# Performance work log

Hardware: AMD Instinct MI355X
Metric: run time of the kernel (lower is better)

The kernel has to match this reference:

```python
import jax, jax.numpy as jnp
import numpy as np

B, S, D, H, FF = 2, 2048, 512, 8, 2048
DK = D // H
EPS = 1e-3  # LayerNorm epsilon from the original module


def _layer_norm(x, gamma, beta):
    # biased variance over last dim, eps added inside sqrt (matches torch var_mean unbiased=False)
    mean = jnp.mean(x, axis=-1, keepdims=True)
    var = jnp.mean(jnp.square(x - mean), axis=-1, keepdims=True)
    return gamma * ((x - mean) / jnp.sqrt(var + EPS)) + beta


def setup_inputs() -> dict:
    key = jax.random.key(0)
    ks = jax.random.split(key, 16)
    sc = 0.02
    p = {
        'x': jax.random.normal(ks[0], (B, S, D), dtype=jnp.float32),
        'lengths': jax.random.randint(ks[1], (B,), 1, S + 1, dtype=jnp.int32),
        'Wq': jax.random.normal(ks[2], (D, D), dtype=jnp.float32) * sc,
        'bq': jnp.zeros((D,), dtype=jnp.float32),
        'Wk': jax.random.normal(ks[3], (D, D), dtype=jnp.float32) * sc,
        'bk': jnp.zeros((D,), dtype=jnp.float32),
        'Wv': jax.random.normal(ks[4], (D, D), dtype=jnp.float32) * sc,
        'bv': jnp.zeros((D,), dtype=jnp.float32),
        'Wo': jax.random.normal(ks[5], (D, D), dtype=jnp.float32) * sc,
        'bo': jnp.zeros((D,), dtype=jnp.float32),
        'W1': jax.random.normal(ks[6], (D, FF), dtype=jnp.float32) * sc,
        'b1': jnp.zeros((FF,), dtype=jnp.float32),
        'W2': jax.random.normal(ks[7], (FF, D), dtype=jnp.float32) * sc,
        'b2': jnp.zeros((D,), dtype=jnp.float32),
        'gamma1': jnp.ones((D,), dtype=jnp.float32),
        'beta1': jnp.zeros((D,), dtype=jnp.float32),
        'gamma2': jnp.ones((D,), dtype=jnp.float32),
        'beta2': jnp.zeros((D,), dtype=jnp.float32),
    }
    return p


def reference(x, lengths, Wq, bq, Wk, bk, Wv, bv, Wo, bo, W1, b1, W2, b2, gamma1, beta1, gamma2, beta2):
    neg_inf = jnp.float32(-jnp.inf)
    pos = jnp.arange(S)
    # pad mask: zero out padded token embeddings (create_pad_mask)
    pad = (pos[None, :] < lengths[:, None]).astype(x.dtype)  # (B, S)
    x = x * pad[:, :, None]

    # hand-rolled multi-head attention (NO 1/sqrt(d_k) scaling, matches original)
    q = (x @ Wq + bq).reshape(B, S, H, DK)
    k = (x @ Wk + bk).reshape(B, S, H, DK)
    v = (x @ Wv + bv).reshape(B, S, H, DK)
    scores = jnp.einsum('bshd,bqhd->bhsq', q, k)  # (B, H, S_query, S_key)

    # causal mask: key col j allowed iff j <= query row i
    causal = pos[None, :] <= pos[:, None]  # (S, S)
    # padding mask: key col j allowed iff j < lengths[b]
    keep = causal[None, None, :, :] & (pos[None, None, None, :] < lengths[:, None, None, None])
    scores = jnp.where(keep, scores, neg_inf)
    attn = jax.nn.softmax(scores, axis=-1)  # (B, H, S, S)

    # FAITHFUL to torch.einsum('bhss,bshd->bshd'): repeated 's' takes the DIAGONAL
    diag = jnp.einsum('bhss->bhs', attn)  # (B, H, S)
    weighted = diag.transpose(0, 2, 1)[:, :, :, None] * v  # (B, S, H, DK)
    attn_out = weighted.reshape(B, S, D) @ Wo + bo

    x = _layer_norm(x + attn_out, gamma1, beta1)
    ff = jax.nn.relu(x @ W1 + b1) @ W2 + b2  # dropout is identity in eval
    x = _layer_norm(x + ff, gamma2, beta2)
    return x
```

## Files before the change

kernel.cpp:

```cpp
#include <hip/hip_runtime.h>

#define B_   2
#define S_   2048
#define D_   512
#define H_   8
#define DK_  64
#define FF_  2048
#define EPS_ 1e-3f
#define QS_  1536

typedef __bf16 bf16;
typedef __bf16 bf16x4 __attribute__((ext_vector_type(4)));
typedef __bf16 bf16x8 __attribute__((ext_vector_type(8)));
typedef float  f32x4  __attribute__((ext_vector_type(4)));

__device__ __forceinline__ void gload16(const bf16* g, bf16* l) {
  __builtin_amdgcn_global_load_lds(
      (__attribute__((address_space(1))) void*)g,
      (__attribute__((address_space(3))) void*)l, 16, 0, 0);
}

struct PrepArgs {
  const float* w[4];
  bf16* thi[4];
  bf16* tlo[4];
  int rowOff[4];
  const float* W1; bf16* W1hi; bf16* W1lo;
  const float* W2; bf16* W2hi; bf16* W2lo;
  const float* x; const int* lengths; bf16* xhi; bf16* xlo;
  const float* bq; const float* bk; const float* bv; float* bqkv;
};

__device__ __forceinline__ void transpose_tile(const float* W, int K, int N,
                                               bf16* Thi, bf16* Tlo,
                                               int n0, int k0, int rowOff,
                                               float (*tl)[33], int t) {
  const int tx = t & 31, ty = t >> 5;
#pragma unroll
  for (int r = 0; r < 32; r += 8)
    tl[r + ty][tx] = W[(size_t)(k0 + r + ty) * N + n0 + tx];
  __syncthreads();
#pragma unroll
  for (int r = 0; r < 32; r += 8) {
    const int n = r + ty;
    const float v = tl[tx][n];
    const bf16 h = (bf16)v;
    const size_t o = (size_t)(rowOff + n0 + n) * K + k0 + tx;
    Thi[o] = h;
    Tlo[o] = (bf16)(v - (float)h);
  }
}

__global__ __launch_bounds__(256) void prep_kernel(PrepArgs a) {
  __shared__ float tl[32][33];
  const int id = blockIdx.x;
  const int t = threadIdx.x;
  if (id < 1024) {
    const int wsel = id >> 8, rem = id & 255;
    transpose_tile(a.w[wsel], 512, 512, a.thi[wsel], a.tlo[wsel],
                   (rem & 15) * 32, (rem >> 4) * 32, a.rowOff[wsel], tl, t);
  } else if (id < 2048) {
    const int rem = id - 1024;
    transpose_tile(a.W1, 512, 2048, a.W1hi, a.W1lo,
                   (rem & 63) * 32, (rem >> 6) * 32, 0, tl, t);
  } else if (id < 3072) {
    const int rem = id - 2048;
    transpose_tile(a.W2, 2048, 512, a.W2hi, a.W2lo,
                   (rem & 15) * 32, (rem >> 4) * 32, 0, tl, t);
  } else if (id < 5120) {
    const int idx = (id - 3072) * 256 + t;
    const int d4 = D_ / 4;
    const int s = (idx / d4) & (S_ - 1);
    const int b = idx / (d4 * S_);
    float4 v = reinterpret_cast<const float4*>(a.x)[idx];
    if (s >= a.lengths[b]) { v.x = 0.f; v.y = 0.f; v.z = 0.f; v.w = 0.f; }
    const float vv[4] = {v.x, v.y, v.z, v.w};
    bf16x4 h, l;
#pragma unroll
    for (int c = 0; c < 4; ++c) {
      const bf16 hh = (bf16)vv[c];
      h[c] = hh;
      l[c] = (bf16)(vv[c] - (float)hh);
    }
    reinterpret_cast<bf16x4*>(a.xhi)[idx] = h;
    reinterpret_cast<bf16x4*>(a.xlo)[idx] = l;
  } else {
    const int i = (id - 5120) * 256 + t;
    if (i < 1536)
      a.bqkv[i] = (i < 512) ? a.bq[i] : (i < 1024) ? a.bk[i - 512] : a.bv[i - 1024];
  }
}

enum { EPI_BIAS_RELU = 2, EPI_PART = 4, EPI_QKV = 5 };

template <int EPI, bool SPLIT, int BN>
__global__ __launch_bounds__(256) void gemm_kernel(
    const bf16* __restrict__ Ahi, const bf16* __restrict__ Alo,
    const bf16* __restrict__ Bhi, const bf16* __restrict__ Blo,
    const float* __restrict__ bias,
    float* __restrict__ C, float* __restrict__ C2,
    bf16* __restrict__ Chi, bf16* __restrict__ Clo,
    int K, int ldc, int nx, int mn, int ksplit) {
  constexpr int NR = BN / 32;
  __shared__ __align__(16) bf16 As[2][128][32];
  __shared__ __align__(16) bf16 Bs[2][BN][32];
  const int t = threadIdx.x;

  const int nwg = gridDim.x;
  const int chunk = nwg >> 3;
  const int virt = (blockIdx.x & 7) * chunk + (blockIdx.x >> 3);
  const int s = virt / mn;
  const int v2 = virt - s * mn;
  const int m0 = (v2 / nx) * 128, n0 = (v2 % nx) * BN;
  const int kb = s * ksplit;

  const int lane = t & 63, wv = t >> 6;
  const int fr = lane & 15, fg = lane >> 4;
  const int wm = (wv >> 1) * 64, wn = (wv & 1) * (BN / 2);
  const int sr = lane >> 2, sslot = lane & 3;

  f32x4 acc[4][NR] = {};

  const bf16* gAh = Ahi + (size_t)m0 * K + kb;
  const bf16* gAl = Alo + (size_t)m0 * K + kb;
  const bf16* gBh = Bhi + (size_t)n0 * K + kb;
  const bf16* gBl = Blo + (size_t)n0 * K + kb;

  for (int k0 = 0; k0 < ksplit; k0 += 32) {
#pragma unroll
    for (int q = 0; q < 2; ++q) {
      const int r = wv * 32 + q * 16 + sr;
      const size_t go = (size_t)r * K + k0 + sslot * 8;
      gload16(gAh + go, &As[0][wv * 32 + q * 16][0]);
      gload16(gAl + go, &As[1][wv * 32 + q * 16][0]);
    }
    if constexpr (BN == 128) {
#pragma unroll
      for (int q = 0; q < 2; ++q) {
        const int r = wv * 32 + q * 16 + sr;
        const size_t go = (size_t)r * K + k0 + sslot * 8;
        gload16(gBh + go, &Bs[0][wv * 32 + q * 16][0]);
        gload16(gBl + go, &Bs[1][wv * 32 + q * 16][0]);
      }
    } else {
      const int r = wv * 16 + sr;
      const size_t go = (size_t)r * K + k0 + sslot * 8;
      gload16(gBh + go, &Bs[0][wv * 16][0]);
      gload16(gBl + go, &Bs[1][wv * 16][0]);
    }
    __syncthreads();

    bf16x8 ah[4], al[4], bh[NR], bl[NR];
#pragma unroll
    for (int m = 0; m < 4; ++m) {
      const int r = wm + m * 16 + fr;
      ah[m] = *reinterpret_cast<const bf16x8*>(&As[0][r][fg * 8]);
      al[m] = *reinterpret_cast<const bf16x8*>(&As[1][r][fg * 8]);
    }
#pragma unroll
    for (int n = 0; n < NR; ++n) {
      const int r = wn + n * 16 + fr;
      bh[n] = *reinterpret_cast<const bf16x8*>(&Bs[0][r][fg * 8]);
      bl[n] = *reinterpret_cast<const bf16x8*>(&Bs[1][r][fg * 8]);
    }
#pragma unroll
    for (int m = 0; m < 4; ++m)
#pragma unroll
      for (int n = 0; n < NR; ++n) {
        acc[m][n] = __builtin_amdgcn_mfma_f32_16x16x32_bf16(bh[n], ah[m], acc[m][n], 0, 0, 0);
        acc[m][n] = __builtin_amdgcn_mfma_f32_16x16x32_bf16(bl[n], ah[m], acc[m][n], 0, 0, 0);
        acc[m][n] = __builtin_amdgcn_mfma_f32_16x16x32_bf16(bh[n], al[m], acc[m][n], 0, 0, 0);
      }
    __syncthreads();
  }

  float* __restrict__ Cw = (s == 0) ? C : C2;
#pragma unroll
  for (int m = 0; m < 4; ++m) {
    const int row = m0 + wm + m * 16 + fr;
#pragma unroll
    for (int n = 0; n < NR; ++n) {
      const int col = n0 + wn + n * 16 + fg * 4;
      f32x4 v = acc[m][n];
      if constexpr (EPI != EPI_PART) {
        const f32x4 b4 = *reinterpret_cast<const f32x4*>(bias + col);
#pragma unroll
        for (int c = 0; c < 4; ++c) v[c] += b4[c];
      }
      if constexpr (EPI == EPI_BIAS_RELU) {
#pragma unroll
        for (int c = 0; c < 4; ++c) v[c] = fmaxf(v[c], 0.f);
      }
      if constexpr (EPI == EPI_QKV) {
        if (col < 1024) {
          bf16x4 h, l;
#pragma unroll
          for (int c = 0; c < 4; ++c) {
            const bf16 hh = (bf16)v[c];
            h[c] = hh;
            l[c] = (bf16)(v[c] - (float)hh);
          }
          *reinterpret_cast<bf16x4*>(&Chi[(size_t)row * 1024 + col]) = h;
          *reinterpret_cast<bf16x4*>(&Clo[(size_t)row * 1024 + col]) = l;
        } else {
          *reinterpret_cast<f32x4*>(&C[(size_t)row * D_ + col - 1024]) = v;
        }
      } else if constexpr (SPLIT) {
        bf16x4 h, l;
#pragma unroll
        for (int c = 0; c < 4; ++c) {
          const bf16 hh = (bf16)v[c];
          h[c] = hh;
          l[c] = (bf16)(v[c] - (float)hh);
        }
        *reinterpret_cast<bf16x4*>(&Chi[(size_t)row * ldc + col]) = h;
        *reinterpret_cast<bf16x4*>(&Clo[(size_t)row * ldc + col]) = l;
      } else {
        *reinterpret_cast<f32x4*>(&Cw[(size_t)row * ldc + col]) = v;
      }
    }
  }
}

__global__ __launch_bounds__(256) void attn_part_kernel(
    const bf16* __restrict__ qk_hi, const bf16* __restrict__ qk_lo,
    const int* __restrict__ lengths,
    float* __restrict__ pm, float* __restrict__ pl, float* __restrict__ pd) {
  __shared__ __align__(16) bf16 Qh[64][72], Ql[64][72];
  __shared__ __align__(16) bf16 Kh[64][72], Kl[64][72];
  const int t = threadIdx.x;
  const int lane = t & 63, wv = t >> 6;
  const int fr = lane & 15, fg = lane >> 4;
  const int bh = blockIdx.y;
  const int bb = bh >> 3, h = bh & 7;

  const int p = blockIdx.x;
  int a = (int)sqrtf((float)p);
  while ((a + 1) * (a + 1) <= p) ++a;
  while (a * a > p) --a;
  int ib, jc;
  if (p >= a * a + a) { ib = 2 * a;     jc = p - (a * a + a); }
  else                { ib = 2 * a - 1; jc = p - a * a; }

  const int i0 = ib * 64;
  const int len = lengths[bb];
  if (i0 >= len || jc * 128 >= len) return;

  const int sr = t >> 2, sc0 = (t & 3) * 16;
  {
    const size_t gb = (size_t)(bb * S_ + i0 + sr) * 1024 + h * DK_ + sc0;
    *reinterpret_cast<int4*>(&Qh[sr][sc0])     = *reinterpret_cast<const int4*>(qk_hi + gb);
    *reinterpret_cast<int4*>(&Qh[sr][sc0 + 8]) = *reinterpret_cast<const int4*>(qk_hi + gb + 8);
    *reinterpret_cast<int4*>(&Ql[sr][sc0])     = *reinterpret_cast<const int4*>(qk_lo + gb);
    *reinterpret_cast<int4*>(&Ql[sr][sc0 + 8]) = *reinterpret_cast<const int4*>(qk_lo + gb + 8);
  }

  float m_r[4], l_r[4], d_r[4];
#pragma unroll
  for (int r = 0; r < 4; ++r) { m_r[r] = -1e30f; l_r[r] = 0.f; d_r[r] = 0.f; }

  const int jlim = min(i0 + 63, len - 1);
  for (int jt = 0; jt < 2; ++jt) {
    const int j0 = jc * 128 + jt * 64;
    if (j0 > jlim) break;
    {
      const size_t gb = (size_t)(bb * S_ + j0 + sr) * 1024 + 512 + h * DK_ + sc0;
      *reinterpret_cast<int4*>(&Kh[sr][sc0])     = *reinterpret_cast<const int4*>(qk_hi + gb);
      *reinterpret_cast<int4*>(&Kh[sr][sc0 + 8]) = *reinterpret_cast<const int4*>(qk_hi + gb + 8);
      *reinterpret_cast<int4*>(&Kl[sr][sc0])     = *reinterpret_cast<const int4*>(qk_lo + gb);
      *reinterpret_cast<int4*>(&Kl[sr][sc0 + 8]) = *reinterpret_cast<const int4*>(qk_lo + gb + 8);
    }
    __syncthreads();

    f32x4 sc[4] = {};
#pragma unroll
    for (int kk = 0; kk < 2; ++kk) {
      const bf16x8 qh = *reinterpret_cast<const bf16x8*>(&Qh[wv * 16 + fr][kk * 32 + fg * 8]);
      const bf16x8 ql = *reinterpret_cast<const bf16x8*>(&Ql[wv * 16 + fr][kk * 32 + fg * 8]);
#pragma unroll
      for (int jf = 0; jf < 4; ++jf) {
        const bf16x8 kh = *reinterpret_cast<const bf16x8*>(&Kh[jf * 16 + fr][kk * 32 + fg * 8]);
        const bf16x8 kl = *reinterpret_cast<const bf16x8*>(&Kl[jf * 16 + fr][kk * 32 + fg * 8]);
        sc[jf] = __builtin_amdgcn_mfma_f32_16x16x32_bf16(qh, kh, sc[jf], 0, 0, 0);
        sc[jf] = __builtin_amdgcn_mfma_f32_16x16x32_bf16(qh, kl, sc[jf], 0, 0, 0);
        sc[jf] = __builtin_amdgcn_mfma_f32_16x16x32_bf16(ql, kh, sc[jf], 0, 0, 0);
      }
    }

#pragma unroll
    for (int r = 0; r < 4; ++r) {
      const int ig = i0 + wv * 16 + fg * 4 + r;
      float s4[4];
      float mx = -1e30f;
#pragma unroll
      for (int jf = 0; jf < 4; ++jf) {
        const int j = j0 + jf * 16 + fr;
        float v = sc[jf][r];
        if (j > ig || j >= len) v = -1e30f;
        s4[jf] = v;
        mx = fmaxf(mx, v);
      }
#pragma unroll
      for (int off = 1; off < 16; off <<= 1) mx = fmaxf(mx, __shfl_xor(mx, off));
      const float mnew = fmaxf(m_r[r], mx);
      float ps = 0.f, pdg = 0.f;
#pragma unroll
      for (int jf = 0; jf < 4; ++jf) {
        const float e = __expf(s4[jf] - mnew);
        ps += e;
        if (j0 + jf * 16 + fr == ig) pdg = e;
      }
#pragma unroll
      for (int off = 1; off < 16; off <<= 1) {
        ps += __shfl_xor(ps, off);
        pdg += __shfl_xor(pdg, off);
      }
      const float scale = __expf(m_r[r] - mnew);
      l_r[r] = l_r[r] * scale + ps;
      d_r[r] = d_r[r] * scale + pdg;
      m_r[r] = mnew;
    }
    __syncthreads();
  }

  if (fr == 0) {
    const size_t base = ((size_t)(bh * 32 + ib) * 16 + jc) * 64;
#pragma unroll
    for (int r = 0; r < 4; ++r) {
      const int row = wv * 16 + fg * 4 + r;
      const float mm = m_r[r];
      const bool ok = mm > -1e29f;
      pm[base + row] = mm;
      pl[base + row] = ok ? l_r[r] : 0.f;
      pd[base + row] = ok ? d_r[r] : 0.f;
    }
  }
}

__global__ __launch_bounds__(256) void attn_merge_kernel(
    const float* __restrict__ vsrc, const int* __restrict__ lengths,
    const float* __restrict__ pm, const float* __restrict__ pl,
    const float* __restrict__ pd, bf16* __restrict__ whi, bf16* __restrict__ wlo) {
  __shared__ float msh[4][64], lsh[4][64], dsh[4][64];
  __shared__ float dgs[64];
  const int t = threadIdx.x;
  const int ib = blockIdx.x, bh = blockIdx.y;
  const int bb = bh >> 3, h = bh & 7;
  const int i0 = ib * 64;
  const int len = lengths[bb];

  const int r = t & 63, g = t >> 6;
  float m = -1e30f, l = 0.f, d = 0.f;
  if (i0 < len) {
    const int jcmax = min((i0 + 63) >> 7, (len - 1) >> 7);
    const size_t base = ((size_t)(bh * 32 + ib) * 16) * 64 + r;
    for (int jc = g; jc <= jcmax; jc += 4) {
      const size_t idx = base + (size_t)jc * 64;
      const float m2 = pm[idx], l2 = pl[idx], d2 = pd[idx];
      const float mn = fmaxf(m, m2);
      const float e1 = __expf(m - mn), e2 = __expf(m2 - mn);
      l = l * e1 + l2 * e2;
      d = d * e1 + d2 * e2;
      m = mn;
    }
  }
  msh[g][r] = m; lsh[g][r] = l; dsh[g][r] = d;
  __syncthreads();
  if (t < 64) {
    float M = msh[0][t], L = lsh[0][t], Dv = dsh[0][t];
#pragma unroll
    for (int gg = 1; gg < 4; ++gg) {
      const float m2 = msh[gg][t], l2 = lsh[gg][t], d2 = dsh[gg][t];
      const float mn = fmaxf(M, m2);
      const float e1 = __expf(M - mn), e2 = __expf(m2 - mn);
      L = L * e1 + l2 * e2;
      Dv = Dv * e1 + d2 * e2;
      M = mn;
    }
    dgs[t] = (i0 + t < len) ? Dv / L : 0.f;
  }
  __syncthreads();

  const int rr = t >> 2, q = t & 3;
  const float dg = dgs[rr];
  const size_t obase = (size_t)(bb * S_ + i0 + rr) * D_ + h * DK_;
#pragma unroll
  for (int kk = 0; kk < 4; ++kk) {
    const int col = q * 4 + kk * 16;
    const float4 v4 = *reinterpret_cast<const float4*>(vsrc + obase + col);
    const float vv[4] = {dg * v4.x, dg * v4.y, dg * v4.z, dg * v4.w};
    bf16x4 hh, ll;
#pragma unroll
    for (int c = 0; c < 4; ++c) {
      const bf16 x = (bf16)vv[c];
      hh[c] = x;
      ll[c] = (bf16)(vv[c] - (float)x);
    }
    *reinterpret_cast<bf16x4*>(&whi[obase + col]) = hh;
    *reinterpret_cast<bf16x4*>(&wlo[obase + col]) = ll;
  }
}

__global__ __launch_bounds__(256) void ln1_fused_kernel(
    const float* __restrict__ P0, const float* __restrict__ P1,
    const float* __restrict__ x, const int* __restrict__ lengths,
    const float* __restrict__ bo,
    const float* __restrict__ gamma, const float* __restrict__ beta,
    bf16* __restrict__ Yhi, bf16* __restrict__ Ylo) {
  const int row = blockIdx.x;
  const int t = threadIdx.x;
  const int lenb = lengths[row >> 11];
  const bool valid = (row & (S_ - 1)) < lenb;
  const size_t ro = (size_t)row * D_ + t * 2;
  const float2 p0 = *reinterpret_cast<const float2*>(P0 + ro);
  const float2 p1 = *reinterpret_cast<const float2*>(P1 + ro);
  const float2 xv = *reinterpret_cast<const float2*>(x + ro);
  const float2 bv = *reinterpret_cast<const float2*>(bo + t * 2);
  float hx = p0.x + p1.x + bv.x + (valid ? xv.x : 0.f);
  float hy = p0.y + p1.y + bv.y + (valid ? xv.y : 0.f);

  float s = hx + hy, s2 = hx * hx + hy * hy;
#pragma unroll
  for (int off = 1; off < 64; off <<= 1) {
    s += __shfl_xor(s, off);
    s2 += __shfl_xor(s2, off);
  }
  __shared__ float red[8];
  const int w = t >> 6;
  if ((t & 63) == 0) { red[w] = s; red[4 + w] = s2; }
  __syncthreads();
  const float ts  = red[0] + red[1] + red[2] + red[3];
  const float ts2 = red[4] + red[5] + red[6] + red[7];
  const float mean = ts * (1.f / D_);
  const float var  = ts2 * (1.f / D_) - mean * mean;
  const float inv  = 1.f / sqrtf(var + EPS_);
  const float2 g  = *reinterpret_cast<const float2*>(gamma + t * 2);
  const float2 bt = *reinterpret_cast<const float2*>(beta + t * 2);
  const float ox = g.x * ((hx - mean) * inv) + bt.x;
  const float oy = g.y * ((hy - mean) * inv) + bt.y;
  const bf16 ohx = (bf16)ox, ohy = (bf16)oy;
  Yhi[ro] = ohx;  Yhi[ro + 1] = ohy;
  Ylo[ro] = (bf16)(ox - (float)ohx);
  Ylo[ro + 1] = (bf16)(oy - (float)ohy);
}

__global__ __launch_bounds__(256) void ln2_fused_kernel(
    const float* __restrict__ Q0, const float* __restrict__ Q1,
    const bf16* __restrict__ Yhi, const bf16* __restrict__ Ylo,
    const float* __restrict__ b2,
    const float* __restrict__ gamma, const float* __restrict__ beta,
    float* __restrict__ out) {
  const int row = blockIdx.x;
  const int t = threadIdx.x;
  const size_t ro = (size_t)row * D_ + t * 2;
  const float2 q0 = *reinterpret_cast<const float2*>(Q0 + ro);
  const float2 q1 = *reinterpret_cast<const float2*>(Q1 + ro);
  const float2 bv = *reinterpret_cast<const float2*>(b2 + t * 2);
  const float y1x = (float)Yhi[ro] + (float)Ylo[ro];
  const float y1y = (float)Yhi[ro + 1] + (float)Ylo[ro + 1];
  float hx = q0.x + q1.x + bv.x + y1x;
  float hy = q0.y + q1.y + bv.y + y1y;

  float s = hx + hy, s2 = hx * hx + hy * hy;
#pragma unroll
  for (int off = 1; off < 64; off <<= 1) {
    s += __shfl_xor(s, off);
    s2 += __shfl_xor(s2, off);
  }
  __shared__ float red[8];
  const int w = t >> 6;
  if ((t & 63) == 0) { red[w] = s; red[4 + w] = s2; }
  __syncthreads();
  const float ts  = red[0] + red[1] + red[2] + red[3];
  const float ts2 = red[4] + red[5] + red[6] + red[7];
  const float mean = ts * (1.f / D_);
  const float var  = ts2 * (1.f / D_) - mean * mean;
  const float inv  = 1.f / sqrtf(var + EPS_);
  const float2 g  = *reinterpret_cast<const float2*>(gamma + t * 2);
  const float2 bt = *reinterpret_cast<const float2*>(beta + t * 2);
  float2 o;
  o.x = g.x * ((hx - mean) * inv) + bt.x;
  o.y = g.y * ((hy - mean) * inv) + bt.y;
  *reinterpret_cast<float2*>(out + ro) = o;
}

extern "C" void kernel_launch(void* const* d_in, const int* in_sizes, int n_in,
                              void* d_out, int out_size, void* d_ws, size_t ws_size,
                              hipStream_t stream) {
  const float* x       = (const float*)d_in[0];
  const int*   lengths = (const int*)d_in[1];
  const float* Wq = (const float*)d_in[2];
  const float* bq = (const float*)d_in[3];
  const float* Wk = (const float*)d_in[4];
  const float* bk = (const float*)d_in[5];
  const float* Wv = (const float*)d_in[6];
  const float* bv = (const float*)d_in[7];
  const float* Wo = (const float*)d_in[8];
  const float* bo = (const float*)d_in[9];
  const float* W1 = (const float*)d_in[10];
  const float* b1 = (const float*)d_in[11];
  const float* W2 = (const float*)d_in[12];
  const float* b2 = (const float*)d_in[13];
  const float* gamma1 = (const float*)d_in[14];
  const float* beta1  = (const float*)d_in[15];
  const float* gamma2 = (const float*)d_in[16];
  const float* beta2  = (const float*)d_in[17];
  float* out = (float*)d_out;

  char* ws = (char*)d_ws;
  bf16*  qkvT_hi = (bf16*)(ws + 0);
  bf16*  qkvT_lo = (bf16*)(ws + 1572864);
  bf16*  WoT_hi  = (bf16*)(ws + 3145728);
  bf16*  WoT_lo  = (bf16*)(ws + 3670016);
  bf16*  W1T_hi  = (bf16*)(ws + 4194304);
  bf16*  W1T_lo  = (bf16*)(ws + 6291456);
  bf16*  W2T_hi  = (bf16*)(ws + 8388608);
  bf16*  W2T_lo  = (bf16*)(ws + 10485760);
  float* bqkv    = (float*)(ws + 12582912);
  bf16*  qk_hi   = (bf16*)(ws + 12589056);
  bf16*  qk_lo   = (bf16*)(ws + 20977664);
  float* v_f32   = (float*)(ws + 29366272);
  float* P0      = (float*)(ws + 12589056);
  float* P1      = (float*)(ws + 20977664);
  float* part_m  = (float*)(ws + 37754880);
  float* part_l  = (float*)(ws + 39852032);
  float* part_d  = (float*)(ws + 41949184);
  bf16*  ff1_hi  = (bf16*)(ws + 12589056);
  bf16*  ff1_lo  = (bf16*)(ws + 29366272);
  bf16*  xm_hi   = (bf16*)(ws + 46143488);
  bf16*  xm_lo   = (bf16*)(ws + 50337792);
  bf16*  y1_hi   = (bf16*)(ws + 46143488);
  bf16*  y1_lo   = (bf16*)(ws + 50337792);
  bf16*  wgt_hi  = (bf16*)(ws + 54532096);
  bf16*  wgt_lo  = (bf16*)(ws + 58726400);
  float* Q0      = (float*)(ws + 54532096);
  float* Q1      = (float*)(ws + 0);

  const dim3 blk(256);
  const int M = B_ * S_;

  PrepArgs pa;
  pa.w[0] = Wq; pa.w[1] = Wk; pa.w[2] = Wv; pa.w[3] = Wo;
  pa.thi[0] = qkvT_hi; pa.thi[1] = qkvT_hi; pa.thi[2] = qkvT_hi; pa.thi[3] = WoT_hi;
  pa.tlo[0] = qkvT_lo; pa.tlo[1] = qkvT_lo; pa.tlo[2] = qkvT_lo; pa.tlo[3] = WoT_lo;
  pa.rowOff[0] = 0; pa.rowOff[1] = 512; pa.rowOff[2] = 1024; pa.rowOff[3] = 0;
  pa.W1 = W1; pa.W1hi = W1T_hi; pa.W1lo = W1T_lo;
  pa.W2 = W2; pa.W2hi = W2T_hi; pa.W2lo = W2T_lo;
  pa.x = x; pa.lengths = lengths; pa.xhi = xm_hi; pa.xlo = xm_lo;
  pa.bq = bq; pa.bk = bk; pa.bv = bv; pa.bqkv = bqkv;
  prep_kernel<<<dim3(5126), blk, 0, stream>>>(pa);

  gemm_kernel<EPI_QKV, false, 64><<<dim3(768), blk, 0, stream>>>(
      xm_hi, xm_lo, qkvT_hi, qkvT_lo, bqkv,
      v_f32, nullptr, qk_hi, qk_lo, 512, QS_, 24, 768, 512);

  attn_part_kernel<<<dim3(272, 16), blk, 0, stream>>>(qk_hi, qk_lo, lengths,
                                                      part_m, part_l, part_d);
  attn_merge_kernel<<<dim3(32, 16), blk, 0, stream>>>(v_f32, lengths, part_m, part_l, part_d,
                                                      wgt_hi, wgt_lo);

  gemm_kernel<EPI_PART, false, 64><<<dim3(512), blk, 0, stream>>>(
      wgt_hi, wgt_lo, WoT_hi, WoT_lo, nullptr,
      P0, P1, nullptr, nullptr, 512, D_, 8, 256, 256);

  ln1_fused_kernel<<<dim3(M), blk, 0, stream>>>(P0, P1, x, lengths, bo,
                                                gamma1, beta1, y1_hi, y1_lo);

  gemm_kernel<EPI_BIAS_RELU, true, 64><<<dim3(1024), blk, 0, stream>>>(
      y1_hi, y1_lo, W1T_hi, W1T_lo, b1,
      nullptr, nullptr, ff1_hi, ff1_lo, 512, FF_, 32, 1024, 512);

  gemm_kernel<EPI_PART, false, 64><<<dim3(512), blk, 0, stream>>>(
      ff1_hi, ff1_lo, W2T_hi, W2T_lo, nullptr,
      Q0, Q1, nullptr, nullptr, FF_, D_, 8, 256, 1024);

  ln2_fused_kernel<<<dim3(M), blk, 0, stream>>>(Q0, Q1, y1_hi, y1_lo, b2,
                                                gamma2, beta2, out);
}
```

Baseline: 260.0 us.

## Double-buffer LDS tiles in split-bf16 GEMM to overlap loads with MFMA

Adds a second LDS buffer for the A and B hi/lo tiles in the GEMM kernel. The global-to-LDS loads for the next k-tile are issued before the MFMA work on the current tile, so memory latency can hide behind compute instead of stalling at the top of each iteration. In exchange LDS use per workgroup doubles, up to 64KB when BN is 128, which may lower occupancy. Correctness relies on the barrier at the end of each iteration also waiting for the outstanding async loads.

```diff
diff --git a/kernel.cpp b/kernel.cpp
--- a/kernel.cpp
+++ b/kernel.cpp
@@ -102,8 +102,8 @@
     bf16* __restrict__ Chi, bf16* __restrict__ Clo,
     int K, int ldc, int nx, int mn, int ksplit) {
   constexpr int NR = BN / 32;
-  __shared__ __align__(16) bf16 As[2][128][32];
-  __shared__ __align__(16) bf16 Bs[2][BN][32];
+  __shared__ __align__(16) bf16 As[2][2][128][32];
+  __shared__ __align__(16) bf16 Bs[2][2][BN][32];
   const int t = threadIdx.x;
 
   const int nwg = gridDim.x;
@@ -126,42 +126,50 @@
   const bf16* gBh = Bhi + (size_t)n0 * K + kb;
   const bf16* gBl = Blo + (size_t)n0 * K + kb;
 
-  for (int k0 = 0; k0 < ksplit; k0 += 32) {
+  auto stage = [&](int buf, int k0) {
 #pragma unroll
     for (int q = 0; q < 2; ++q) {
       const int r = wv * 32 + q * 16 + sr;
       const size_t go = (size_t)r * K + k0 + sslot * 8;
-      gload16(gAh + go, &As[0][wv * 32 + q * 16][0]);
-      gload16(gAl + go, &As[1][wv * 32 + q * 16][0]);
+      gload16(gAh + go, &As[buf][0][wv * 32 + q * 16][0]);
+      gload16(gAl + go, &As[buf][1][wv * 32 + q * 16][0]);
     }
     if constexpr (BN == 128) {
 #pragma unroll
       for (int q = 0; q < 2; ++q) {
         const int r = wv * 32 + q * 16 + sr;
         const size_t go = (size_t)r * K + k0 + sslot * 8;
-        gload16(gBh + go, &Bs[0][wv * 32 + q * 16][0]);
-        gload16(gBl + go, &Bs[1][wv * 32 + q * 16][0]);
+        gload16(gBh + go, &Bs[buf][0][wv * 32 + q * 16][0]);
+        gload16(gBl + go, &Bs[buf][1][wv * 32 + q * 16][0]);
       }
     } else {
       const int r = wv * 16 + sr;
       const size_t go = (size_t)r * K + k0 + sslot * 8;
-      gload16(gBh + go, &Bs[0][wv * 16][0]);
-      gload16(gBl + go, &Bs[1][wv * 16][0]);
-    }
-    __syncthreads();
+      gload16(gBh + go, &Bs[buf][0][wv * 16][0]);
+      gload16(gBl + go, &Bs[buf][1][wv * 16][0]);
+    }
+  };
+
+  const int nt = ksplit >> 5;
+  stage(0, 0);
+  __syncthreads();
+
+  for (int kt = 0; kt < nt; ++kt) {
+    const int cur = kt & 1;
+    if (kt + 1 < nt) stage(cur ^ 1, (kt + 1) << 5);
 
     bf16x8 ah[4], al[4], bh[NR], bl[NR];
 #pragma unroll
     for (int m = 0; m < 4; ++m) {
       const int r = wm + m * 16 + fr;
-      ah[m] = *reinterpret_cast<const bf16x8*>(&As[0][r][fg * 8]);
-      al[m] = *reinterpret_cast<const bf16x8*>(&As[1][r][fg * 8]);
+      ah[m] = *reinterpret_cast<const bf16x8*>(&As[cur][0][r][fg * 8]);
+      al[m] = *reinterpret_cast<const bf16x8*>(&As[cur][1][r][fg * 8]);
     }
 #pragma unroll
     for (int n = 0; n < NR; ++n) {
       const int r = wn + n * 16 + fr;
-      bh[n] = *reinterpret_cast<const bf16x8*>(&Bs[0][r][fg * 8]);
-      bl[n] = *reinterpret_cast<const bf16x8*>(&Bs[1][r][fg * 8]);
+      bh[n] = *reinterpret_cast<const bf16x8*>(&Bs[cur][0][r][fg * 8]);
+      bl[n] = *reinterpret_cast<const bf16x8*>(&Bs[cur][1][r][fg * 8]);
     }
 #pragma unroll
     for (int m = 0; m < 4; ++m)
```

New measurement: 263.8 us. No clear change (+1.4%).
